# Kernel tuning notes

Measured on AMD Instinct MI355X. Metric: run time of the kernel, lower is better.

## Reference

```python
import jax, jax.numpy as jnp
import numpy as np

N = 4096


def setup_inputs() -> dict:
    key = jax.random.key(0)
    ks = jax.random.split(key, 24)

    def idx(k, n, cols):
        base = jax.random.randint(k, (n,), 0, N)
        return jnp.stack([(base + j) % N for j in range(cols)], axis=1).astype(jnp.int32)

    x = jax.random.normal(ks[0], (N, 3), jnp.float32) * 3.0  # spread points so min pair dist is not tiny
    bond = idx(ks[1], 6144, 2)
    kb = jax.random.uniform(ks[2], (6144,), jnp.float32)
    b0 = jax.random.uniform(ks[3], (6144,), jnp.float32)
    angle = idx(ks[4], 8192, 3)
    kt = jax.random.uniform(ks[5], (8192,), jnp.float32)
    t0 = jax.random.uniform(ks[6], (8192,), jnp.float32) * 180.0  # degrees
    ureybradley = idx(ks[7], 4096, 2)
    ku = jax.random.uniform(ks[8], (4096,), jnp.float32)
    s0 = jax.random.uniform(ks[9], (4096,), jnp.float32)
    dihedral = idx(ks[10], 12288, 4)
    kd = jax.random.uniform(ks[11], (12288,), jnp.float32)
    nd = jax.random.randint(ks[12], (12288,), 1, 4).astype(jnp.float32)  # multiplicity
    d0 = jax.random.uniform(ks[13], (12288,), jnp.float32) * 360.0
    improper = idx(ks[14], 2048, 4)
    kp = jax.random.uniform(ks[15], (2048,), jnp.float32)
    p0 = jax.random.uniform(ks[16], (2048,), jnp.float32) * 180.0
    eps_ij = jax.random.uniform(ks[17], (N, N), jnp.float32)
    rmin_ij = jax.random.uniform(ks[18], (N, N), jnp.float32) * 0.5
    kqq_ij = jax.random.normal(ks[19], (N, N), jnp.float32)
    return dict(x=x, kb=kb, b0=b0, kt=kt, t0=t0, ku=ku, s0=s0, kd=kd, nd=nd, d0=d0,
                kp=kp, p0=p0, eps_ij=eps_ij, rmin_ij=rmin_ij, kqq_ij=kqq_ij,
                bond=bond, angle=angle, ureybradley=ureybradley,
                dihedral=dihedral, improper=improper, central=0)


def _torsion(x, quad):
    # signed dihedral angle for [M,4] index quadruples
    ab = x[quad[:, 1]] - x[quad[:, 0]]
    bc = x[quad[:, 2]] - x[quad[:, 1]]
    cd = x[quad[:, 3]] - x[quad[:, 2]]
    n1 = jnp.cross(ab, bc)
    n2 = jnp.cross(bc, cd)
    cos_d = jnp.sum(n1 * n2, axis=1) / (jnp.linalg.norm(n1, axis=1) * jnp.linalg.norm(n2, axis=1))
    ang = jnp.arccos(jnp.clip(cos_d, -0.9999, 0.9999))
    return ang * jnp.sign(jnp.sum(jnp.cross(n1, n2) * bc, axis=1))


def _energy(x, kb, b0, kt, t0, ku, s0, kd, nd, d0, kp, p0,
            eps_ij, rmin_ij, kqq_ij, bond, angle, ureybradley, dihedral, improper, central):
    # bonds
    dis = jnp.linalg.norm(x[bond[:, 0]] - x[bond[:, 1]], axis=1)
    V_bond = jnp.sum(kb * (dis - b0) ** 2)
    # angles
    ba = x[angle[:, 0]] - x[angle[:, 1]]
    bc = x[angle[:, 2]] - x[angle[:, 1]]
    cos_t = jnp.sum(ba * bc, axis=1) / (jnp.linalg.norm(ba, axis=1) * jnp.linalg.norm(bc, axis=1))
    theta = jnp.arccos(jnp.clip(cos_t, -0.9999, 0.9999))
    V_angle = jnp.sum(kt * (theta - jnp.deg2rad(t0)) ** 2)
    # Urey-Bradley 1-3 terms
    dub = jnp.linalg.norm(x[ureybradley[:, 0]] - x[ureybradley[:, 1]], axis=1)
    V_ub = jnp.sum(ku * (dub - s0) ** 2)
    # proper dihedrals
    delta = _torsion(x, dihedral)
    V_dih = jnp.sum(kd * (1.0 + jnp.cos(nd * delta - jnp.deg2rad(d0))))
    # impropers (harmonic)
    psi = _torsion(x, improper)
    V_imp = jnp.sum(kp * (psi - jnp.deg2rad(p0)) ** 2)
    # nonbonded: cdist(x,x) + I, summed over strict upper triangle
    n = x.shape[0]
    sq = jnp.sum(x * x, axis=1)
    d2 = jnp.maximum(sq[:, None] + sq[None, :] - 2.0 * (x @ x.T), 1e-12)
    eye = jnp.eye(n, dtype=bool)
    dist = jnp.sqrt(jnp.where(eye, 1.0, d2))  # diag -> 1, matching cdist + eye
    rod = rmin_ij / dist
    vdw = eps_ij * (rod ** 12 - 2.0 * rod ** 6)
    mask = jnp.triu(jnp.ones((n, n), bool), 1)
    V_vdw = jnp.sum(jnp.where(mask, vdw, 0.0))
    V_ele = jnp.sum(jnp.where(mask, kqq_ij / dist, 0.0))
    V = V_bond + V_angle + V_ub + V_dih + V_imp + V_vdw + V_ele
    if central:
        V = V + jnp.sum(0.1 * jnp.sum((x - jnp.mean(x, axis=0)) ** 2, axis=1))
    return V


def reference(x, kb, b0, kt, t0, ku, s0, kd, nd, d0, kp, p0,
              eps_ij, rmin_ij, kqq_ij, bond, angle, ureybradley, dihedral, improper, central):
    return _energy(x, kb, b0, kt, t0, ku, s0, kd, nd, d0, kp, p0,
                   eps_ij, rmin_ij, kqq_ij, bond, angle, ureybradley, dihedral, improper, central)
```

## Files before the change

### kernel.cpp

```cpp
#include <hip/hip_runtime.h>

#define NATOM   4096
#define NG4     (NATOM / 4)
#define NBOND   6144
#define NANGLE  8192
#define NUB     4096
#define NDIH    12288
#define NIMP    2048

#define NB_BLOCKS   2048
#define BOND_ITEMS  (NBOND + NANGLE + NUB + NDIH + NIMP)
#define BOND_WORKB  (BOND_ITEMS / 256)
#define BOND_BLOCKS (BOND_WORKB + 1)
#define TOTAL_SLOTS (NB_BLOCKS + BOND_BLOCKS)

#define DEG2RAD 0.017453292519943295f

static __device__ __forceinline__ double block_reduce(double v, double* sm) {
    #pragma unroll
    for (int off = 32; off > 0; off >>= 1) v += __shfl_down(v, off, 64);
    const int lane = threadIdx.x & 63, wid = threadIdx.x >> 6;
    __syncthreads();
    if (lane == 0) sm[wid] = v;
    __syncthreads();
    double r = 0.0;
    if (threadIdx.x == 0) {
        const int nw = blockDim.x >> 6;
        for (int w = 0; w < nw; ++w) r += sm[w];
    }
    return r;
}

static __device__ __forceinline__ float pair_term(
    float xi0, float xi1, float xi2,
    float xj0, float xj1, float xj2,
    float e, float r, float q, bool valid)
{
    const float dx = xi0 - xj0, dy = xi1 - xj1, dz = xi2 - xj2;
    float d2 = fmaf(dx, dx, fmaf(dy, dy, dz * dz));
    d2 = fmaxf(d2, 1e-12f);
    float inv = rsqrtf(d2);
    const float t = inv * inv;
    inv = inv * fmaf(-0.5f * d2, t, 1.5f);
    const float rod = r * inv;
    const float r2 = rod * rod;
    const float r6 = r2 * r2 * r2;
    const float v = fmaf(e * r6, r6 - 2.0f, q * inv);
    return valid ? v : 0.0f;
}

static __device__ __forceinline__ float group_term(
    int i, float xi0, float xi1, float xi2, int g,
    float4 e, float4 r, float4 q, float4 xa, float4 xb, float4 xc)
{
    const int j0 = 4 * g;
    float s;
    s  = pair_term(xi0,xi1,xi2, xa.x,xa.y,xa.z, e.x,r.x,q.x, j0+0 > i);
    s += pair_term(xi0,xi1,xi2, xa.w,xb.x,xb.y, e.y,r.y,q.y, j0+1 > i);
    s += pair_term(xi0,xi1,xi2, xb.z,xb.w,xc.x, e.z,r.z,q.z, j0+2 > i);
    s += pair_term(xi0,xi1,xi2, xc.y,xc.z,xc.w, e.w,r.w,q.w, j0+3 > i);
    return s;
}

static __device__ __forceinline__ float torsion(const float* __restrict__ x,
                                                int i0, int i1, int i2, int i3) {
    const float ax = x[3*i1] - x[3*i0], ay = x[3*i1+1] - x[3*i0+1], az = x[3*i1+2] - x[3*i0+2];
    const float bx = x[3*i2] - x[3*i1], by = x[3*i2+1] - x[3*i1+1], bz = x[3*i2+2] - x[3*i1+2];
    const float cx = x[3*i3] - x[3*i2], cy = x[3*i3+1] - x[3*i2+1], cz = x[3*i3+2] - x[3*i2+2];
    const float n1x = ay*bz - az*by, n1y = az*bx - ax*bz, n1z = ax*by - ay*bx;
    const float n2x = by*cz - bz*cy, n2y = bz*cx - bx*cz, n2z = bx*cy - by*cx;
    const float dt  = n1x*n2x + n1y*n2y + n1z*n2z;
    const float nn1 = sqrtf(n1x*n1x + n1y*n1y + n1z*n1z);
    const float nn2 = sqrtf(n2x*n2x + n2y*n2y + n2z*n2z);
    float c = dt / (nn1 * nn2);
    c = fminf(fmaxf(c, -0.9999f), 0.9999f);
    const float ang = acosf(c);
    const float sx = n1y*n2z - n1z*n2y, sy = n1z*n2x - n1x*n2z, sz = n1x*n2y - n1y*n2x;
    const float s = sx*bx + sy*by + sz*bz;
    const float sg = (s > 0.0f) ? 1.0f : ((s < 0.0f) ? -1.0f : 0.0f);
    return ang * sg;
}

__global__ __launch_bounds__(256) void ff_kernel(
    const float4* __restrict__ xv,
    const float4* __restrict__ eps,
    const float4* __restrict__ rmin,
    const float4* __restrict__ kqq,
    const float* __restrict__ kb, const float* __restrict__ b0,
    const float* __restrict__ kt, const float* __restrict__ t0,
    const float* __restrict__ ku, const float* __restrict__ s0,
    const float* __restrict__ kd, const float* __restrict__ nd, const float* __restrict__ d0,
    const float* __restrict__ kp, const float* __restrict__ p0,
    const int* __restrict__ bond, const int* __restrict__ angle,
    const int* __restrict__ ub,   const int* __restrict__ dih,
    const int* __restrict__ imp,  const int* __restrict__ central,
    double* __restrict__ ws)
{
    __shared__ double sm[4];
    const float* __restrict__ x = (const float*)xv;

    if (blockIdx.x < NB_BLOCKS) {
        const int b = (int)blockIdx.x;
        const int t = (int)threadIdx.x;
        double acc = 0.0;
        #pragma unroll
        for (int half = 0; half < 2; ++half) {
            const int i = half ? (NATOM - 1 - b) : b;
            const float xi0 = x[3*i], xi1 = x[3*i+1], xi2 = x[3*i+2];
            const int g0 = (i + 1) >> 2;
            const size_t rowbase = (size_t)i * NG4;

            int gs[4]; bool ok[4];
            #pragma unroll
            for (int u = 0; u < 4; ++u) {
                const int g = g0 + t + (u << 8);
                ok[u] = (g < NG4);
                gs[u] = ok[u] ? g : (NG4 - 1);
            }
            float4 le[4], lr[4], lq[4];
            #pragma unroll
            for (int u = 0; u < 4; ++u) le[u] = eps [rowbase + gs[u]];
            #pragma unroll
            for (int u = 0; u < 4; ++u) lr[u] = rmin[rowbase + gs[u]];
            #pragma unroll
            for (int u = 0; u < 4; ++u) lq[u] = kqq [rowbase + gs[u]];
            #pragma unroll
            for (int u = 0; u < 4; ++u) {
                const int g3 = 3 * gs[u];
                const float4 xa = xv[g3], xb = xv[g3+1], xc = xv[g3+2];
                const float s = group_term(i, xi0, xi1, xi2, gs[u],
                                           le[u], lr[u], lq[u], xa, xb, xc);
                acc += (double)(ok[u] ? s : 0.0f);
            }
        }
        const double tot = block_reduce(acc, sm);
        if (t == 0) ws[blockIdx.x] = tot;
        return;
    }

    const int bb = (int)blockIdx.x - NB_BLOCKS;

    if (bb == BOND_WORKB) {
        double out = 0.0;
        if (*central != 0) {
            double sx = 0.0, sy = 0.0, sz = 0.0, s2 = 0.0;
            for (int i = threadIdx.x; i < NATOM; i += 256) {
                const float a = x[3*i], b = x[3*i+1], c = x[3*i+2];
                sx += a; sy += b; sz += c;
                s2 += (double)a*a + (double)b*b + (double)c*c;
            }
            const double rx = block_reduce(sx, sm);
            const double ry = block_reduce(sy, sm);
            const double rz = block_reduce(sz, sm);
            const double r2 = block_reduce(s2, sm);
            if (threadIdx.x == 0)
                out = 0.1 * (r2 - (rx*rx + ry*ry + rz*rz) / (double)NATOM);
        }
        if (threadIdx.x == 0) ws[NB_BLOCKS + bb] = out;
        return;
    }

    const int t = bb * 256 + (int)threadIdx.x;
    double v = 0.0;

    if (t < NBOND) {
        const int m = t;
        const int i = bond[2*m], j = bond[2*m+1];
        const float dx = x[3*i]-x[3*j], dy = x[3*i+1]-x[3*j+1], dz = x[3*i+2]-x[3*j+2];
        const float dis = sqrtf(dx*dx + dy*dy + dz*dz);
        const float d = dis - b0[m];
        v = (double)(kb[m] * d * d);
    } else if (t < NBOND + NANGLE) {
        const int m = t - NBOND;
        const int i = angle[3*m], j = angle[3*m+1], k = angle[3*m+2];
        const float bax = x[3*i]-x[3*j], bay = x[3*i+1]-x[3*j+1], baz = x[3*i+2]-x[3*j+2];
        const float bcx = x[3*k]-x[3*j], bcy = x[3*k+1]-x[3*j+1], bcz = x[3*k+2]-x[3*j+2];
        const float dt  = bax*bcx + bay*bcy + baz*bcz;
        const float na  = sqrtf(bax*bax + bay*bay + baz*baz);
        const float nb  = sqrtf(bcx*bcx + bcy*bcy + bcz*bcz);
        float c = dt / (na * nb);
        c = fminf(fmaxf(c, -0.9999f), 0.9999f);
        const float theta = acosf(c);
        const float d = theta - t0[m] * DEG2RAD;
        v = (double)(kt[m] * d * d);
    } else if (t < NBOND + NANGLE + NUB) {
        const int m = t - NBOND - NANGLE;
        const int i = ub[2*m], j = ub[2*m+1];
        const float dx = x[3*i]-x[3*j], dy = x[3*i+1]-x[3*j+1], dz = x[3*i+2]-x[3*j+2];
        const float dis = sqrtf(dx*dx + dy*dy + dz*dz);
        const float d = dis - s0[m];
        v = (double)(ku[m] * d * d);
    } else if (t < NBOND + NANGLE + NUB + NDIH) {
        const int m = t - NBOND - NANGLE - NUB;
        const float delta = torsion(x, dih[4*m], dih[4*m+1], dih[4*m+2], dih[4*m+3]);
        v = (double)(kd[m] * (1.0f + cosf(nd[m] * delta - d0[m] * DEG2RAD)));
    } else {
        const int m = t - NBOND - NANGLE - NUB - NDIH;
        const float psi = torsion(x, imp[4*m], imp[4*m+1], imp[4*m+2], imp[4*m+3]);
        const float d = psi - p0[m] * DEG2RAD;
        v = (double)(kp[m] * d * d);
    }

    const double tot = block_reduce(v, sm);
    if (threadIdx.x == 0) ws[NB_BLOCKS + bb] = tot;
}

__global__ __launch_bounds__(256) void finalize_kernel(const double* __restrict__ ws,
                                                       float* __restrict__ out) {
    __shared__ double sm[4];
    double v = 0.0;
    for (int i = threadIdx.x; i < TOTAL_SLOTS; i += 256) v += ws[i];
    const double tot = block_reduce(v, sm);
    if (threadIdx.x == 0) out[0] = (float)tot;
}

extern "C" void kernel_launch(void* const* d_in, const int* in_sizes, int n_in,
                              void* d_out, int out_size, void* d_ws, size_t ws_size,
                              hipStream_t stream) {
    const float* x    = (const float*)d_in[0];
    const float* kb   = (const float*)d_in[1];
    const float* b0   = (const float*)d_in[2];
    const float* kt   = (const float*)d_in[3];
    const float* t0   = (const float*)d_in[4];
    const float* ku   = (const float*)d_in[5];
    const float* s0   = (const float*)d_in[6];
    const float* kd   = (const float*)d_in[7];
    const float* nd   = (const float*)d_in[8];
    const float* d0   = (const float*)d_in[9];
    const float* kp   = (const float*)d_in[10];
    const float* p0   = (const float*)d_in[11];
    const float* eps  = (const float*)d_in[12];
    const float* rmin = (const float*)d_in[13];
    const float* kqq  = (const float*)d_in[14];
    const int* bond   = (const int*)d_in[15];
    const int* angle  = (const int*)d_in[16];
    const int* ub     = (const int*)d_in[17];
    const int* dih    = (const int*)d_in[18];
    const int* imp    = (const int*)d_in[19];
    const int* cent   = (const int*)d_in[20];

    double* ws = (double*)d_ws;

    ff_kernel<<<NB_BLOCKS + BOND_BLOCKS, 256, 0, stream>>>(
        (const float4*)x, (const float4*)eps, (const float4*)rmin, (const float4*)kqq,
        kb, b0, kt, t0, ku, s0, kd, nd, d0, kp, p0,
        bond, angle, ub, dih, imp, cent, ws);
    finalize_kernel<<<1, 256, 0, stream>>>(ws, (float*)d_out);
}
```

Measured before the change: 215.3 us.

## Stage atom coordinates in shared memory as SoA for nonbonded blocks

Each nonbonded block now copies the slice of atom coordinates it needs from global memory into three shared-memory arrays (x, y, z), so the j-atom positions come from shared memory as one float4 per component instead of three global float4 loads. The per-row loop also drops the fixed 4-way unrolled batch of eps/rmin/kqq loads and runs a variable-count loop over only the groups in range. This aims to cut redundant global and L2 traffic for coordinates and wasted clamped loads. In exchange it adds 48KB of static shared memory per block, which lowers occupancy for every block, bond blocks included, plus a barrier and a strided staging loop that uses integer division. The runtime loop bound may also reduce memory-level parallelism.

```diff
diff --git a/kernel.cpp b/kernel.cpp
--- a/kernel.cpp
+++ b/kernel.cpp
@@ -51,14 +51,14 @@
 
 static __device__ __forceinline__ float group_term(
     int i, float xi0, float xi1, float xi2, int g,
-    float4 e, float4 r, float4 q, float4 xa, float4 xb, float4 xc)
+    float4 e, float4 r, float4 q, float4 px, float4 py, float4 pz)
 {
     const int j0 = 4 * g;
     float s;
-    s  = pair_term(xi0,xi1,xi2, xa.x,xa.y,xa.z, e.x,r.x,q.x, j0+0 > i);
-    s += pair_term(xi0,xi1,xi2, xa.w,xb.x,xb.y, e.y,r.y,q.y, j0+1 > i);
-    s += pair_term(xi0,xi1,xi2, xb.z,xb.w,xc.x, e.z,r.z,q.z, j0+2 > i);
-    s += pair_term(xi0,xi1,xi2, xc.y,xc.z,xc.w, e.w,r.w,q.w, j0+3 > i);
+    s  = pair_term(xi0,xi1,xi2, px.x,py.x,pz.x, e.x,r.x,q.x, j0+0 > i);
+    s += pair_term(xi0,xi1,xi2, px.y,py.y,pz.y, e.y,r.y,q.y, j0+1 > i);
+    s += pair_term(xi0,xi1,xi2, px.z,py.z,pz.z, e.z,r.z,q.z, j0+2 > i);
+    s += pair_term(xi0,xi1,xi2, px.w,py.w,pz.w, e.w,r.w,q.w, j0+3 > i);
     return s;
 }
 
@@ -82,10 +82,10 @@
 }
 
 __global__ __launch_bounds__(256) void ff_kernel(
-    const float4* __restrict__ xv,
     const float4* __restrict__ eps,
     const float4* __restrict__ rmin,
     const float4* __restrict__ kqq,
+    const float* __restrict__ x,
     const float* __restrict__ kb, const float* __restrict__ b0,
     const float* __restrict__ kt, const float* __restrict__ t0,
     const float* __restrict__ ku, const float* __restrict__ s0,
@@ -97,40 +97,50 @@
     double* __restrict__ ws)
 {
     __shared__ double sm[4];
-    const float* __restrict__ x = (const float*)xv;
+    __shared__ __align__(16) float sx[NATOM];
+    __shared__ __align__(16) float sy[NATOM];
+    __shared__ __align__(16) float sz[NATOM];
 
     if (blockIdx.x < NB_BLOCKS) {
         const int b = (int)blockIdx.x;
         const int t = (int)threadIdx.x;
+        const int i0 = b, i1 = NATOM - 1 - b;
+        const int g0a = (i0 + 1) >> 2, g0b = (i1 + 1) >> 2;
+        const float xi00 = x[3*i0], xi01 = x[3*i0+1], xi02 = x[3*i0+2];
+        const float xi10 = x[3*i1], xi11 = x[3*i1+1], xi12 = x[3*i1+2];
+
+        for (int e = 12 * g0a + t; e < 3 * NATOM; e += 256) {
+            const float v = x[e];
+            const int a = e / 3, c = e - 3 * a;
+            if (c == 0)      sx[a] = v;
+            else if (c == 1) sy[a] = v;
+            else             sz[a] = v;
+        }
+        __syncthreads();
+
         double acc = 0.0;
         #pragma unroll
         for (int half = 0; half < 2; ++half) {
-            const int i = half ? (NATOM - 1 - b) : b;
-            const float xi0 = x[3*i], xi1 = x[3*i+1], xi2 = x[3*i+2];
-            const int g0 = (i + 1) >> 2;
+            const int i  = half ? i1 : i0;
+            const int g0 = half ? g0b : g0a;
+            const float xi0c = half ? xi10 : xi00;
+            const float xi1c = half ? xi11 : xi01;
+            const float xi2c = half ? xi12 : xi02;
             const size_t rowbase = (size_t)i * NG4;
-
-            int gs[4]; bool ok[4];
-            #pragma unroll
-            for (int u = 0; u < 4; ++u) {
+            const int umax = (NG4 - g0 + 255) >> 8;
+            for (int u = 0; u < umax; ++u) {
                 const int g = g0 + t + (u << 8);
-                ok[u] = (g < NG4);
-                gs[u] = ok[u] ? g : (NG4 - 1);
-            }
-            float4 le[4], lr[4], lq[4];
-            #pragma unroll
-            for (int u = 0; u < 4; ++u) le[u] = eps [rowbase + gs[u]];
-            #pragma unroll
-            for (int u = 0; u < 4; ++u) lr[u] = rmin[rowbase + gs[u]];
-            #pragma unroll
-            for (int u = 0; u < 4; ++u) lq[u] = kqq [rowbase + gs[u]];
-            #pragma unroll
-            for (int u = 0; u < 4; ++u) {
-                const int g3 = 3 * gs[u];
-                const float4 xa = xv[g3], xb = xv[g3+1], xc = xv[g3+2];
-                const float s = group_term(i, xi0, xi1, xi2, gs[u],
-                                           le[u], lr[u], lq[u], xa, xb, xc);
-                acc += (double)(ok[u] ? s : 0.0f);
+                const bool ok = (g < NG4);
+                const int gc = ok ? g : (NG4 - 1);
+                const float4 e4 = eps [rowbase + gc];
+                const float4 r4 = rmin[rowbase + gc];
+                const float4 q4 = kqq [rowbase + gc];
+                const float4 px = *(const float4*)&sx[4*gc];
+                const float4 py = *(const float4*)&sy[4*gc];
+                const float4 pz = *(const float4*)&sz[4*gc];
+                const float s = group_term(i, xi0c, xi1c, xi2c, gc,
+                                           e4, r4, q4, px, py, pz);
+                acc += (double)(ok ? s : 0.0f);
             }
         }
         const double tot = block_reduce(acc, sm);
@@ -143,15 +153,15 @@
     if (bb == BOND_WORKB) {
         double out = 0.0;
         if (*central != 0) {
-            double sx = 0.0, sy = 0.0, sz = 0.0, s2 = 0.0;
+            double sxx = 0.0, syy = 0.0, szz = 0.0, s2 = 0.0;
             for (int i = threadIdx.x; i < NATOM; i += 256) {
                 const float a = x[3*i], b = x[3*i+1], c = x[3*i+2];
-                sx += a; sy += b; sz += c;
+                sxx += a; syy += b; szz += c;
                 s2 += (double)a*a + (double)b*b + (double)c*c;
             }
-            const double rx = block_reduce(sx, sm);
-            const double ry = block_reduce(sy, sm);
-            const double rz = block_reduce(sz, sm);
+            const double rx = block_reduce(sxx, sm);
+            const double ry = block_reduce(syy, sm);
+            const double rz = block_reduce(szz, sm);
             const double r2 = block_reduce(s2, sm);
             if (threadIdx.x == 0)
                 out = 0.1 * (r2 - (rx*rx + ry*ry + rz*rz) / (double)NATOM);
@@ -242,7 +252,7 @@
     double* ws = (double*)d_ws;
 
     ff_kernel<<<NB_BLOCKS + BOND_BLOCKS, 256, 0, stream>>>(
-        (const float4*)x, (const float4*)eps, (const float4*)rmin, (const float4*)kqq,
+        (const float4*)eps, (const float4*)rmin, (const float4*)kqq, x,
         kb, b0, kt, t0, ku, s0, kd, nd, d0, kp, p0,
         bond, angle, ub, dih, imp, cent, ws);
     finalize_kernel<<<1, 256, 0, stream>>>(ws, (float*)d_out);
```

Result: slower. 229.4 us (+6.5%).

## Process four rows per block to share x-column loads across rows

Applied to the files above, without the earlier changes.

Each nonbonded block now handles four rows (two adjacent rows from each end of the triangle) instead of two, and loops over column groups with each thread loading the column atom coordinates once and reusing them for all four rows. The block count is halved, and the blocks are interleaved so front and back block indices alternate. This aims to cut the redundant x loads and give each thread more independent work, but it replaces the fully unrolled batch of twelve independent matrix loads with a loop that has only three loads in flight per row step, which may reduce memory-level parallelism on this bandwidth-bound sweep.

```diff
diff --git a/kernel.cpp b/kernel.cpp
--- a/kernel.cpp
+++ b/kernel.cpp
@@ -8,11 +8,11 @@
 #define NDIH    12288
 #define NIMP    2048
 
-#define NB_BLOCKS   2048
+#define NBPAIR  1024
 #define BOND_ITEMS  (NBOND + NANGLE + NUB + NDIH + NIMP)
 #define BOND_WORKB  (BOND_ITEMS / 256)
 #define BOND_BLOCKS (BOND_WORKB + 1)
-#define TOTAL_SLOTS (NB_BLOCKS + BOND_BLOCKS)
+#define TOTAL_SLOTS (NBPAIR + BOND_BLOCKS)
 
 #define DEG2RAD 0.017453292519943295f
 
@@ -82,10 +82,10 @@
 }
 
 __global__ __launch_bounds__(256) void ff_kernel(
-    const float4* __restrict__ xv,
     const float4* __restrict__ eps,
     const float4* __restrict__ rmin,
     const float4* __restrict__ kqq,
+    const float4* __restrict__ xv,
     const float* __restrict__ kb, const float* __restrict__ b0,
     const float* __restrict__ kt, const float* __restrict__ t0,
     const float* __restrict__ ku, const float* __restrict__ s0,
@@ -99,38 +99,45 @@
     __shared__ double sm[4];
     const float* __restrict__ x = (const float*)xv;
 
-    if (blockIdx.x < NB_BLOCKS) {
-        const int b = (int)blockIdx.x;
+    if (blockIdx.x < NBPAIR) {
+        const int m = (int)blockIdx.x;
+        const int b = (m & 1) ? (NBPAIR - 1 - (m >> 1)) : (m >> 1);
         const int t = (int)threadIdx.x;
+
+        int   irow[4];
+        irow[0] = 2 * b;
+        irow[1] = 2 * b + 1;
+        irow[2] = NATOM - 2 - 2 * b;
+        irow[3] = NATOM - 1 - 2 * b;
+
+        float xi[4][3]; int grow0[4]; size_t rowbase[4];
+        #pragma unroll
+        for (int r = 0; r < 4; ++r) {
+            const int i = irow[r];
+            xi[r][0] = x[3*i]; xi[r][1] = x[3*i+1]; xi[r][2] = x[3*i+2];
+            grow0[r] = (i + 1) >> 2;
+            rowbase[r] = (size_t)i * NG4;
+        }
+        const int g_min = grow0[0];
+
         double acc = 0.0;
-        #pragma unroll
-        for (int half = 0; half < 2; ++half) {
-            const int i = half ? (NATOM - 1 - b) : b;
-            const float xi0 = x[3*i], xi1 = x[3*i+1], xi2 = x[3*i+2];
-            const int g0 = (i + 1) >> 2;
-            const size_t rowbase = (size_t)i * NG4;
-
-            int gs[4]; bool ok[4];
+        for (int gb = g_min; gb < NG4; gb += 256) {
+            const int g  = gb + t;
+            const bool ok = (g < NG4);
+            const int gc = ok ? g : (NG4 - 1);
+            const int g3 = 3 * gc;
+            const float4 xa = xv[g3], xb = xv[g3+1], xc = xv[g3+2];
             #pragma unroll
-            for (int u = 0; u < 4; ++u) {
-                const int g = g0 + t + (u << 8);
-                ok[u] = (g < NG4);
-                gs[u] = ok[u] ? g : (NG4 - 1);
-            }
-            float4 le[4], lr[4], lq[4];
-            #pragma unroll
-            for (int u = 0; u < 4; ++u) le[u] = eps [rowbase + gs[u]];
-            #pragma unroll
-            for (int u = 0; u < 4; ++u) lr[u] = rmin[rowbase + gs[u]];
-            #pragma unroll
-            for (int u = 0; u < 4; ++u) lq[u] = kqq [rowbase + gs[u]];
-            #pragma unroll
-            for (int u = 0; u < 4; ++u) {
-                const int g3 = 3 * gs[u];
-                const float4 xa = xv[g3], xb = xv[g3+1], xc = xv[g3+2];
-                const float s = group_term(i, xi0, xi1, xi2, gs[u],
-                                           le[u], lr[u], lq[u], xa, xb, xc);
-                acc += (double)(ok[u] ? s : 0.0f);
+            for (int r = 0; r < 4; ++r) {
+                if (gb + 255 >= grow0[r]) {
+                    const size_t base = rowbase[r] + gc;
+                    const float4 e4 = eps [base];
+                    const float4 r4 = rmin[base];
+                    const float4 q4 = kqq [base];
+                    const float s = group_term(irow[r], xi[r][0], xi[r][1], xi[r][2],
+                                               gc, e4, r4, q4, xa, xb, xc);
+                    acc += (double)(ok ? s : 0.0f);
+                }
             }
         }
         const double tot = block_reduce(acc, sm);
@@ -138,25 +145,25 @@
         return;
     }
 
-    const int bb = (int)blockIdx.x - NB_BLOCKS;
+    const int bb = (int)blockIdx.x - NBPAIR;
 
     if (bb == BOND_WORKB) {
         double out = 0.0;
         if (*central != 0) {
-            double sx = 0.0, sy = 0.0, sz = 0.0, s2 = 0.0;
+            double sxx = 0.0, syy = 0.0, szz = 0.0, s2 = 0.0;
             for (int i = threadIdx.x; i < NATOM; i += 256) {
                 const float a = x[3*i], b = x[3*i+1], c = x[3*i+2];
-                sx += a; sy += b; sz += c;
+                sxx += a; syy += b; szz += c;
                 s2 += (double)a*a + (double)b*b + (double)c*c;
             }
-            const double rx = block_reduce(sx, sm);
-            const double ry = block_reduce(sy, sm);
-            const double rz = block_reduce(sz, sm);
+            const double rx = block_reduce(sxx, sm);
+            const double ry = block_reduce(syy, sm);
+            const double rz = block_reduce(szz, sm);
             const double r2 = block_reduce(s2, sm);
             if (threadIdx.x == 0)
                 out = 0.1 * (r2 - (rx*rx + ry*ry + rz*rz) / (double)NATOM);
         }
-        if (threadIdx.x == 0) ws[NB_BLOCKS + bb] = out;
+        if (threadIdx.x == 0) ws[NBPAIR + bb] = out;
         return;
     }
 
@@ -202,7 +209,7 @@
     }
 
     const double tot = block_reduce(v, sm);
-    if (threadIdx.x == 0) ws[NB_BLOCKS + bb] = tot;
+    if (threadIdx.x == 0) ws[NBPAIR + bb] = tot;
 }
 
 __global__ __launch_bounds__(256) void finalize_kernel(const double* __restrict__ ws,
@@ -241,8 +248,8 @@
 
     double* ws = (double*)d_ws;
 
-    ff_kernel<<<NB_BLOCKS + BOND_BLOCKS, 256, 0, stream>>>(
-        (const float4*)x, (const float4*)eps, (const float4*)rmin, (const float4*)kqq,
+    ff_kernel<<<NBPAIR + BOND_BLOCKS, 256, 0, stream>>>(
+        (const float4*)eps, (const float4*)rmin, (const float4*)kqq, (const float4*)x,
         kb, b0, kt, t0, ku, s0, kd, nd, d0, kp, p0,
         bond, angle, ub, dih, imp, cent, ws);
     finalize_kernel<<<1, 256, 0, stream>>>(ws, (float*)d_out);
```

Result: no change. 217.5 us (+1.0%).
